# Performance work log

Measured on AMD Instinct MI355X. Metric: run time of the kernel, lower is better.

## Reference

```python
import jax, jax.numpy as jnp
import numpy as np

HEADS = 8
DIM_HEAD = 64
DIM = 512
MAX_POS_EMB = 512
SCALE = DIM_HEAD ** -0.5


def setup_inputs() -> dict:
    key = jax.random.key(0)
    ks = jax.random.split(key, 6)
    B, N = 2, 2048
    inner = HEADS * DIM_HEAD  # 512
    x = jax.random.normal(ks[0], (B, N, DIM), dtype=jnp.float32)
    # torch Linear weights stored as [out, in]; we keep [in, out] for x @ W
    Wq = jax.random.normal(ks[1], (DIM, inner), dtype=jnp.float32) * (DIM ** -0.5)
    Wkv = jax.random.normal(ks[2], (DIM, 2 * inner), dtype=jnp.float32) * (DIM ** -0.5)
    Wo = jax.random.normal(ks[3], (inner, DIM), dtype=jnp.float32) * (inner ** -0.5)
    bo = jax.random.normal(ks[4], (DIM,), dtype=jnp.float32) * 0.02
    rel_emb = jax.random.normal(ks[5], (2 * MAX_POS_EMB + 1, DIM_HEAD), dtype=jnp.float32)
    return {"x": x, "Wq": Wq, "Wkv": Wkv, "Wo": Wo, "bo": bo, "rel_emb": rel_emb}


def reference(x, Wq, Wkv, Wo, bo, rel_emb):
    B, N, _ = x.shape
    h, d = HEADS, DIM_HEAD
    q = x @ Wq                                # [B, N, h*d]
    kv = x @ Wkv                              # [B, N, 2*h*d]
    k, v = jnp.split(kv, 2, axis=-1)
    to_heads = lambda t: t.reshape(B, N, h, d).transpose(0, 2, 1, 3)  # [B, h, N, d]
    q, k, v = to_heads(q), to_heads(k), to_heads(v)

    dots = jnp.einsum('bhid,bhjd->bhij', q, k) * SCALE  # [B, h, N, N]

    # relative positional bias: dist clamped to [-max, max], shifted to [0, 2*max]
    seq = jnp.arange(N)
    dist = jnp.clip(seq[:, None] - seq[None, :], -MAX_POS_EMB, MAX_POS_EMB) + MAX_POS_EMB
    rel = rel_emb[dist]                                 # [N, N, d]
    pos_attn = jnp.einsum('bhnd,njd->bhnj', q, rel) * SCALE
    dots = dots + pos_attn

    attn = jax.nn.softmax(dots, axis=-1)
    out = jnp.einsum('bhij,bhjd->bhid', attn, v)        # [B, h, N, d]
    out = out.transpose(0, 2, 1, 3).reshape(B, N, h * d)
    return out @ Wo + bo
```

## Files before the change

kernel.cpp:

```cpp
#include <hip/hip_runtime.h>
#include <hip/hip_bf16.h>
#include <stdint.h>

#define HEADS 8
#define DHEAD 64
#define DIM 512
#define NSEQ 2048
#define BATCH 2
#define NROWS (BATCH * NSEQ)
#define QKV_N 1536
#define REL_ROWS 1025
#define REL_PITCH_ROWS 1088
#define NSPLIT 2
#define KV_PER_SPLIT (NSEQ / NSPLIT)

static constexpr float SCALE_LOG2E = 0.125f * 1.4426950408889634f;

typedef __attribute__((ext_vector_type(8))) short bf16x8;
typedef __attribute__((ext_vector_type(4))) float f32x4;

__device__ __forceinline__ uint16_t f2bf(float f) {
    union { float f; uint32_t u; } v{f};
    uint32_t r = (v.u + 0x7FFFu + ((v.u >> 16) & 1u)) >> 16;
    return (uint16_t)r;
}

__global__ void prep_all(const float* __restrict__ x, const float* __restrict__ rel,
                         const float* __restrict__ Wq, const float* __restrict__ Wkv,
                         const float* __restrict__ Wo,
                         uint16_t* __restrict__ xb, uint16_t* __restrict__ relb,
                         uint16_t* __restrict__ Wqkv_t, uint16_t* __restrict__ Wo_t) {
    if (blockIdx.x < 2048) {
        int total = NROWS * DIM + REL_PITCH_ROWS * DHEAD;
        for (int idx = blockIdx.x * blockDim.x + threadIdx.x; idx < total; idx += 2048 * blockDim.x) {
            if (idx < NROWS * DIM) {
                xb[idx] = f2bf(x[idx]);
            } else {
                int i2 = idx - NROWS * DIM;
                relb[i2] = (i2 < REL_ROWS * DHEAD) ? f2bf(rel[i2]) : (uint16_t)0;
            }
        }
        return;
    }
    __shared__ float tile[32][33];
    int bid = blockIdx.x - 2048;
    const float* src; uint16_t* dst; int J, ti, tj;
    if (bid < 256)      { src = Wq;  dst = Wqkv_t;             J = 512;  ti = bid >> 4;        tj = bid & 15; }
    else if (bid < 768) { int b = bid - 256; src = Wkv; dst = Wqkv_t + 512 * 512; J = 1024; ti = b >> 5; tj = b & 31; }
    else                { int b = bid - 768; src = Wo;  dst = Wo_t;   J = 512;  ti = b >> 4;        tj = b & 15; }
    int tx = threadIdx.x & 31, ty = threadIdx.x >> 5;
    int k0 = ti * 32, j0 = tj * 32;
    #pragma unroll
    for (int i = 0; i < 4; i++) tile[ty + 8 * i][tx] = src[(size_t)(k0 + ty + 8 * i) * J + j0 + tx];
    __syncthreads();
    #pragma unroll
    for (int i = 0; i < 4; i++) dst[(size_t)(j0 + ty + 8 * i) * 512 + k0 + tx] = f2bf(tile[tx][ty + 8 * i]);
}

template <bool BF16_OUT>
__global__ __launch_bounds__(256) void gemm128(const uint16_t* __restrict__ A,
                                               const uint16_t* __restrict__ Bt,
                                               void* __restrict__ Cout,
                                               const float* __restrict__ bias,
                                               int K, int ldc) {
    __shared__ char lds[32768];
    char* ldsA = lds;
    char* ldsB = lds + 16384;
    int m0 = blockIdx.x * 128, n0 = blockIdx.y * 128;
    int t = threadIdx.x, lane = t & 63, w = t >> 6;
    int wr = w >> 1, wc = w & 1;
    int l15 = lane & 15, lh = lane >> 4;
    f32x4 acc[4][4] = {};
    for (int k0 = 0; k0 < K; k0 += 64) {
        __syncthreads();
        {
            int row = t >> 3, ch = t & 7;
            #pragma unroll
            for (int p = 0; p < 4; p++) {
                int r = row + 32 * p;
                bf16x8 va = *(const bf16x8*)(A + (size_t)(m0 + r) * K + k0 + ch * 8);
                *(bf16x8*)(ldsA + r * 128 + ((ch * 16) ^ ((r & 7) << 4))) = va;
                bf16x8 vb = *(const bf16x8*)(Bt + (size_t)(n0 + r) * K + k0 + ch * 8);
                *(bf16x8*)(ldsB + r * 128 + ((ch * 16) ^ ((r & 7) << 4))) = vb;
            }
        }
        __syncthreads();
        #pragma unroll
        for (int kk = 0; kk < 2; kk++) {
            bf16x8 a[4], b[4];
            #pragma unroll
            for (int mi = 0; mi < 4; mi++) {
                int m = wr * 64 + mi * 16 + l15;
                a[mi] = *(const bf16x8*)(ldsA + m * 128 + ((kk * 64 + lh * 16) ^ ((m & 7) << 4)));
            }
            #pragma unroll
            for (int ni = 0; ni < 4; ni++) {
                int n = wc * 64 + ni * 16 + l15;
                b[ni] = *(const bf16x8*)(ldsB + n * 128 + ((kk * 64 + lh * 16) ^ ((n & 7) << 4)));
            }
            #pragma unroll
            for (int mi = 0; mi < 4; mi++)
                #pragma unroll
                for (int ni = 0; ni < 4; ni++)
                    acc[mi][ni] = __builtin_amdgcn_mfma_f32_16x16x32_bf16(a[mi], b[ni], acc[mi][ni], 0, 0, 0);
        }
    }
    #pragma unroll
    for (int mi = 0; mi < 4; mi++)
        #pragma unroll
        for (int ni = 0; ni < 4; ni++)
            #pragma unroll
            for (int i = 0; i < 4; i++) {
                int m = m0 + wr * 64 + mi * 16 + lh * 4 + i;
                int n = n0 + wc * 64 + ni * 16 + l15;
                float v = acc[mi][ni][i];
                if constexpr (BF16_OUT) ((uint16_t*)Cout)[(size_t)m * ldc + n] = f2bf(v);
                else                    ((float*)Cout)[(size_t)m * ldc + n] = v + bias[n];
            }
}

__global__ __launch_bounds__(512, 4) void attn_kernel(const uint16_t* __restrict__ QKV,
                                                      const uint16_t* __restrict__ relb,
                                                      float* __restrict__ Opart,
                                                      float* __restrict__ mlpart) {
    __shared__ __align__(16) char lds[53248];
    char* ldsQ = lds;
    char* ldsKV = lds + 16384;

    int flat = blockIdx.x + 16 * (blockIdx.y + 8 * blockIdx.z);
    int x = (flat & 7) * 64 + (flat >> 3);
    int qb = x & 15, h = (x >> 4) & 7, z = x >> 7;
    int b = z >> 1, sp = z & 1;

    int t = threadIdx.x, lane = t & 63, w = t >> 6;
    int l15 = lane & 15, lh = lane >> 4;
    int row = t >> 3, ch = t & 7;
    int n0 = qb * 128;
    int kvbase = sp * KV_PER_SPLIT;
    size_t rowQ = (size_t)b * NSEQ + n0;

    int swzSrc = (ch * 16) ^ ((row & 7) << 4);

    #pragma unroll
    for (int p = 0; p < 2; p++) {
        int r = row + 64 * p;
        const char* gsrc = (const char*)(QKV + (rowQ + r) * QKV_N + h * 64)
                           + ((ch * 16) ^ ((r & 7) << 4));
        __builtin_amdgcn_global_load_lds(gsrc, ldsQ + p * 8192 + t * 16, 16, 0, 0);
    }

    {
        int buf = t >> 8, idx = t & 255;
        uint32_t val = (idx < 16) ? 0x3F803F80u : 0u;
        char* p = ldsKV + buf * 18432 + 8192 + 8192 + (idx >> 4) * 128 + (idx & 15) * 8;
        *(uint32_t*)(p) = val;
        *(uint32_t*)(p + 4) = val;
    }

    auto stage_k = [&](int tile) {
        const char* gsrc = (const char*)(QKV + ((size_t)b * NSEQ + kvbase + tile * 64 + row) * QKV_N
                                         + 512 + h * 64) + swzSrc;
        __builtin_amdgcn_global_load_lds(gsrc, ldsKV + (tile & 1) * 18432 + t * 16, 16, 0, 0);
    };
    auto load_v = [&](int tile, bf16x8& vr) {
        vr = *(const bf16x8*)(QKV + ((size_t)b * NSEQ + kvbase + tile * 64 + row) * QKV_N
                              + 1024 + h * 64 + ch * 8);
    };
    auto scatter_v = [&](int tile, bf16x8& vr) {
        char* ldsV = ldsKV + (tile & 1) * 18432 + 8192;
        #pragma unroll
        for (int dd = 0; dd < 8; dd++) {
            int d = ch * 8 + dd;
            int s = dd ^ ch;
            *(uint16_t*)(ldsV + d * 128 + 2 * (row ^ (s << 3))) = (uint16_t)vr[dd];
        }
    };

    bf16x8 vr;
    stage_k(0);
    load_v(0, vr);
    scatter_v(0, vr);
    __syncthreads();

    bf16x8 qf[2];
    #pragma unroll
    for (int kk = 0; kk < 2; kk++) {
        int m = w * 16 + l15;
        qf[kk] = *(const bf16x8*)(ldsQ + m * 128 + ((kk * 64 + lh * 16) ^ ((m & 7) << 4)));
    }
    char* myP = ldsQ + w * 2048;

    f32x4 biasLo = {}, biasHi = {};
    {
        bf16x8 bl0 = *(const bf16x8*)(relb + lh * 8);
        bf16x8 bl1 = *(const bf16x8*)(relb + lh * 8 + 32);
        bf16x8 bh0 = *(const bf16x8*)(relb + 1024 * 64 + lh * 8);
        bf16x8 bh1 = *(const bf16x8*)(relb + 1024 * 64 + lh * 8 + 32);
        biasLo = __builtin_amdgcn_mfma_f32_16x16x32_bf16(qf[0], bl0, biasLo, 0, 0, 0);
        biasLo = __builtin_amdgcn_mfma_f32_16x16x32_bf16(qf[1], bl1, biasLo, 0, 0, 0);
        biasHi = __builtin_amdgcn_mfma_f32_16x16x32_bf16(qf[0], bh0, biasHi, 0, 0, 0);
        biasHi = __builtin_amdgcn_mfma_f32_16x16x32_bf16(qf[1], bh1, biasHi, 0, 0, 0);
    }

    f32x4 oacc[5] = {};
    float mrow[4];
    #pragma unroll
    for (int i = 0; i < 4; i++) mrow[i] = -INFINITY;

    int exAddr[4];
    #pragma unroll
    for (int i = 0; i < 4; i++)
        exAddr[i] = (((lane & 48) | ((lh * 4 + i + 15 - l15) & 15)) << 2);

    const int NT = KV_PER_SPLIT / 64;

    #pragma unroll 1
    for (int tt = 0; tt < NT; ++tt) {
        char* ldsK = ldsKV + (tt & 1) * 18432;
        char* ldsV = ldsK + 8192;
        if (tt > 0) __syncthreads();
        bool pf = (tt + 1 < NT);
        if (pf) {
            stage_k(tt + 1);
            load_v(tt + 1, vr);
        }

        int nk = n0 + w * 16 - (kvbase + tt * 64);
        bool fullLo = (nk <= -527), fullHi = (nk >= 575);

        f32x4 sacc[4] = {};
        __builtin_amdgcn_s_setprio(1);
        #pragma unroll
        for (int kk = 0; kk < 2; kk++)
            #pragma unroll
            for (int nf = 0; nf < 4; nf++) {
                int n = nf * 16 + l15;
                bf16x8 kfv = *(const bf16x8*)(ldsK + n * 128 + ((kk * 64 + lh * 16) ^ ((n & 7) << 4)));
                sacc[nf] = __builtin_amdgcn_mfma_f32_16x16x32_bf16(qf[kk], kfv, sacc[nf], 0, 0, 0);
            }
        __builtin_amdgcn_s_setprio(0);

        if (fullLo || fullHi) {
            f32x4 bc = fullLo ? biasLo : biasHi;
            #pragma unroll
            for (int nf = 0; nf < 4; nf++)
                #pragma unroll
                for (int i = 0; i < 4; i++)
                    sacc[nf][i] += bc[i];
        } else {
            int dlo = nk - 63;
            bf16x8 rfr[2][2];
            {
                int d = dlo + l15;
                d = d < -512 ? -512 : (d > 512 ? 512 : d);
                const uint16_t* rp = relb + (d + 512) * 64 + lh * 8;
                rfr[0][0] = *(const bf16x8*)(rp);
                rfr[0][1] = *(const bf16x8*)(rp + 32);
            }
            f32x4 rect[5] = {};
            #pragma unroll
            for (int f = 0; f < 5; f++) {
                if (f + 1 < 5) {
                    int d = dlo + (f + 1) * 16 + l15;
                    d = d < -512 ? -512 : (d > 512 ? 512 : d);
                    const uint16_t* rp = relb + (d + 512) * 64 + lh * 8;
                    rfr[(f + 1) & 1][0] = *(const bf16x8*)(rp);
                    rfr[(f + 1) & 1][1] = *(const bf16x8*)(rp + 32);
                }
                rect[f] = __builtin_amdgcn_mfma_f32_16x16x32_bf16(qf[0], rfr[f & 1][0], rect[f], 0, 0, 0);
                rect[f] = __builtin_amdgcn_mfma_f32_16x16x32_bf16(qf[1], rfr[f & 1][1], rect[f], 0, 0, 0);
                __builtin_amdgcn_sched_barrier(0);
            }
            #pragma unroll
            for (int i = 0; i < 4; i++) {
                bool hi = (l15 < lh * 4 + i);
                #pragma unroll
                for (int nf = 0; nf < 4; nf++) {
                    float v = hi ? rect[4 - nf][i] : rect[3 - nf][i];
                    union { float f; int s; } un{v};
                    un.s = __builtin_amdgcn_ds_bpermute(exAddr[i], un.s);
                    sacc[nf][i] += un.f;
                }
            }
        }

        float lmax = sacc[0][0];
        #pragma unroll
        for (int nf = 0; nf < 4; nf++)
            #pragma unroll
            for (int i = 0; i < 4; i++) lmax = fmaxf(lmax, sacc[nf][i]);
        float mmin = fminf(fminf(mrow[0], mrow[1]), fminf(mrow[2], mrow[3]));
        if (!__all(lmax <= mmin + 64.0f)) {
            #pragma unroll
            for (int i = 0; i < 4; i++) {
                float mx = fmaxf(fmaxf(sacc[0][i], sacc[1][i]), fmaxf(sacc[2][i], sacc[3][i]));
                mx = fmaxf(mx, __shfl_xor(mx, 1));
                mx = fmaxf(mx, __shfl_xor(mx, 2));
                mx = fmaxf(mx, __shfl_xor(mx, 4));
                mx = fmaxf(mx, __shfl_xor(mx, 8));
                float mnew = fmaxf(mrow[i], mx);
                float alpha = exp2f((mrow[i] - mnew) * SCALE_LOG2E);
                mrow[i] = mnew;
                #pragma unroll
                for (int nf = 0; nf < 5; nf++) oacc[nf][i] *= alpha;
            }
        }

        #pragma unroll
        for (int i = 0; i < 4; i++) {
            int r = lh * 4 + i;
            int rsw = (r & 7) << 4;
            #pragma unroll
            for (int nf = 0; nf < 4; nf++) {
                float p = exp2f((sacc[nf][i] - mrow[i]) * SCALE_LOG2E);
                uint32_t pb;
                asm("v_cvt_pk_bf16_f32 %0, %1, %2" : "=v"(pb) : "v"(p), "v"(p));
                *(uint16_t*)(myP + r * 128 + (((nf * 16 + l15) * 2) ^ rsw)) = (uint16_t)pb;
            }
        }

        asm volatile("s_waitcnt lgkmcnt(0)" ::: "memory");
        __builtin_amdgcn_sched_barrier(0);
        __builtin_amdgcn_s_setprio(1);
        #pragma unroll
        for (int kk = 0; kk < 2; kk++) {
            bf16x8 pa = *(const bf16x8*)(myP + l15 * 128 + ((kk * 64 + lh * 16) ^ ((l15 & 7) << 4)));
            #pragma unroll
            for (int nf = 0; nf < 5; nf++) {
                int d = nf * 16 + l15;
                int sd = (d & 7) ^ ((d >> 3) & 7);
                bf16x8 vb = *(const bf16x8*)(ldsV + d * 128 + 16 * ((kk * 4 + lh) ^ sd));
                oacc[nf] = __builtin_amdgcn_mfma_f32_16x16x32_bf16(pa, vb, oacc[nf], 0, 0, 0);
            }
        }
        __builtin_amdgcn_s_setprio(0);

        if (pf) scatter_v(tt + 1, vr);
        __syncthreads();
    }

    size_t rbase = ((size_t)(sp * BATCH + b) * HEADS + h) * NSEQ;
    #pragma unroll
    for (int nf = 0; nf < 4; nf++)
        #pragma unroll
        for (int i = 0; i < 4; i++) {
            int r = n0 + w * 16 + lh * 4 + i;
            Opart[(rbase + r) * 64 + nf * 16 + l15] = oacc[nf][i];
        }
    if (l15 == 0) {
        #pragma unroll
        for (int i = 0; i < 4; i++) {
            int r = n0 + w * 16 + lh * 4 + i;
            mlpart[(rbase + r) * 2]     = mrow[i];
            mlpart[(rbase + r) * 2 + 1] = oacc[4][i];
        }
    }
}

__global__ __launch_bounds__(256) void combine_kernel(const float* __restrict__ Opart,
                                                      const float* __restrict__ mlpart,
                                                      uint16_t* __restrict__ attO) {
    int lane = threadIdx.x & 63;
    int R = blockIdx.x * 4 + (threadIdx.x >> 6);
    const int SPSTRIDE = BATCH * HEADS * NSEQ;
    float m1 = mlpart[(size_t)R * 2], l1 = mlpart[(size_t)R * 2 + 1];
    float m2 = mlpart[((size_t)SPSTRIDE + R) * 2], l2 = mlpart[((size_t)SPSTRIDE + R) * 2 + 1];
    float M = fmaxf(m1, m2);
    float w1 = exp2f((m1 - M) * SCALE_LOG2E);
    float w2 = exp2f((m2 - M) * SCALE_LOG2E);
    float Linv = 1.f / (l1 * w1 + l2 * w2);
    float o1 = Opart[(size_t)R * 64 + lane];
    float o2 = Opart[((size_t)SPSTRIDE + R) * 64 + lane];
    float o = (o1 * w1 + o2 * w2) * Linv;
    int bh = R >> 11, n = R & 2047;
    int b = bh >> 3, hh = bh & 7;
    attO[((size_t)(b * NSEQ + n)) * DIM + hh * 64 + lane] = f2bf(o);
}

extern "C" void kernel_launch(void* const* d_in, const int* in_sizes, int n_in,
                              void* d_out, int out_size, void* d_ws, size_t ws_size,
                              hipStream_t stream) {
    const float* x   = (const float*)d_in[0];
    const float* Wq  = (const float*)d_in[1];
    const float* Wkv = (const float*)d_in[2];
    const float* Wo  = (const float*)d_in[3];
    const float* bo  = (const float*)d_in[4];
    const float* rel = (const float*)d_in[5];
    char* ws = (char*)d_ws;
    float*    mlp    = (float*)(ws);
    uint16_t* Wo_t   = (uint16_t*)(ws + 524288);
    uint16_t* relb   = (uint16_t*)(ws + 1048576);
    uint16_t* attO   = (uint16_t*)(ws + 1310720);
    uint16_t* QKV    = (uint16_t*)(ws + 5505024);
    float*    Opart  = (float*)(ws + 18087936);
    uint16_t* Xb     = (uint16_t*)(ws + 18087936);
    uint16_t* Wqkv_t = (uint16_t*)(ws + 22282240);

    prep_all<<<3072, 256, 0, stream>>>(x, rel, Wq, Wkv, Wo, Xb, relb, Wqkv_t, Wo_t);
    gemm128<true><<<dim3(32, 12), 256, 0, stream>>>(Xb, Wqkv_t, QKV, nullptr, 512, QKV_N);
    attn_kernel<<<dim3(16, 8, 4), 512, 0, stream>>>(QKV, relb, Opart, mlp);
    combine_kernel<<<8192, 256, 0, stream>>>(Opart, mlp, attO);
    gemm128<false><<<dim3(32, 4), 256, 0, stream>>>(attO, Wo_t, (float*)d_out, bo, 512, DIM);
}
```

Before: 134.0 us.

## Halve attention block to 64 query rows and single-buffer K/V tiles

The attention kernel now uses 256-thread blocks covering 64 query rows instead of 512 threads covering 128, which doubles the grid. K/V LDS staging goes from double-buffered to single-buffered, with the next tile's K load and V scatter issued after the end-of-iteration barrier. Together these cut LDS per block roughly in half, so more blocks can be resident per CU and there are more blocks to spread across the device. The cost is that each K/V tile is reused by fewer query rows, so global traffic rises, and the loss of double buffering exposes load latency within each iteration.

```diff
diff --git a/kernel.cpp b/kernel.cpp
--- a/kernel.cpp
+++ b/kernel.cpp
@@ -119,67 +119,70 @@
             }
 }
 
-__global__ __launch_bounds__(512, 4) void attn_kernel(const uint16_t* __restrict__ QKV,
+__global__ __launch_bounds__(256, 4) void attn_kernel(const uint16_t* __restrict__ QKV,
                                                       const uint16_t* __restrict__ relb,
                                                       float* __restrict__ Opart,
                                                       float* __restrict__ mlpart) {
-    __shared__ __align__(16) char lds[53248];
+    __shared__ __align__(16) char lds[26624];
     char* ldsQ = lds;
-    char* ldsKV = lds + 16384;
-
-    int flat = blockIdx.x + 16 * (blockIdx.y + 8 * blockIdx.z);
-    int x = (flat & 7) * 64 + (flat >> 3);
-    int qb = x & 15, h = (x >> 4) & 7, z = x >> 7;
+    char* ldsK = lds + 8192;
+    char* ldsV = lds + 16384;
+
+    int flat = blockIdx.x + 32 * (blockIdx.y + 8 * blockIdx.z);
+    int x = (flat & 7) * 128 + (flat >> 3);
+    int qb = x & 31, h = (x >> 5) & 7, z = x >> 8;
     int b = z >> 1, sp = z & 1;
 
     int t = threadIdx.x, lane = t & 63, w = t >> 6;
     int l15 = lane & 15, lh = lane >> 4;
-    int row = t >> 3, ch = t & 7;
-    int n0 = qb * 128;
+    int r4 = t >> 2, q4 = t & 3;
+    int n0 = qb * 64;
     int kvbase = sp * KV_PER_SPLIT;
-    size_t rowQ = (size_t)b * NSEQ + n0;
-
-    int swzSrc = (ch * 16) ^ ((row & 7) << 4);
 
     #pragma unroll
     for (int p = 0; p < 2; p++) {
-        int r = row + 64 * p;
-        const char* gsrc = (const char*)(QKV + (rowQ + r) * QKV_N + h * 64)
-                           + ((ch * 16) ^ ((r & 7) << 4));
-        __builtin_amdgcn_global_load_lds(gsrc, ldsQ + p * 8192 + t * 16, 16, 0, 0);
+        int r = p * 32 + (t >> 3);
+        const char* gsrc = (const char*)(QKV + ((size_t)b * NSEQ + n0 + r) * QKV_N + h * 64)
+                           + (((t & 7) * 16) ^ ((r & 7) << 4));
+        __builtin_amdgcn_global_load_lds(gsrc, ldsQ + p * 4096 + t * 16, 16, 0, 0);
     }
 
     {
-        int buf = t >> 8, idx = t & 255;
-        uint32_t val = (idx < 16) ? 0x3F803F80u : 0u;
-        char* p = ldsKV + buf * 18432 + 8192 + 8192 + (idx >> 4) * 128 + (idx & 15) * 8;
+        uint32_t val = ((t >> 4) == 0) ? 0x3F803F80u : 0u;
+        char* p = ldsV + 8192 + (t >> 4) * 128 + (t & 15) * 8;
         *(uint32_t*)(p) = val;
         *(uint32_t*)(p + 4) = val;
     }
 
     auto stage_k = [&](int tile) {
-        const char* gsrc = (const char*)(QKV + ((size_t)b * NSEQ + kvbase + tile * 64 + row) * QKV_N
-                                         + 512 + h * 64) + swzSrc;
-        __builtin_amdgcn_global_load_lds(gsrc, ldsKV + (tile & 1) * 18432 + t * 16, 16, 0, 0);
+        #pragma unroll
+        for (int p = 0; p < 2; p++) {
+            int r = p * 32 + (t >> 3);
+            const char* gsrc = (const char*)(QKV + ((size_t)b * NSEQ + kvbase + tile * 64 + r) * QKV_N
+                                             + 512 + h * 64) + (((t & 7) * 16) ^ ((r & 7) << 4));
+            __builtin_amdgcn_global_load_lds(gsrc, ldsK + p * 4096 + t * 16, 16, 0, 0);
+        }
     };
-    auto load_v = [&](int tile, bf16x8& vr) {
-        vr = *(const bf16x8*)(QKV + ((size_t)b * NSEQ + kvbase + tile * 64 + row) * QKV_N
-                              + 1024 + h * 64 + ch * 8);
+    auto load_v = [&](int tile, bf16x8* vr) {
+        size_t gro = ((size_t)b * NSEQ + kvbase + tile * 64 + r4) * QKV_N + 1024 + h * 64 + q4 * 16;
+        vr[0] = *(const bf16x8*)(QKV + gro);
+        vr[1] = *(const bf16x8*)(QKV + gro + 8);
     };
-    auto scatter_v = [&](int tile, bf16x8& vr) {
-        char* ldsV = ldsKV + (tile & 1) * 18432 + 8192;
-        #pragma unroll
-        for (int dd = 0; dd < 8; dd++) {
-            int d = ch * 8 + dd;
-            int s = dd ^ ch;
-            *(uint16_t*)(ldsV + d * 128 + 2 * (row ^ (s << 3))) = (uint16_t)vr[dd];
-        }
+    auto scatter_v = [&](bf16x8* vr) {
+        #pragma unroll
+        for (int p = 0; p < 2; p++)
+            #pragma unroll
+            for (int dd = 0; dd < 8; dd++) {
+                int d = q4 * 16 + p * 8 + dd;
+                int s = (d & 7) ^ (d >> 3);
+                *(uint16_t*)(ldsV + d * 128 + 2 * (r4 ^ (s << 3))) = (uint16_t)vr[p][dd];
+            }
     };
 
-    bf16x8 vr;
+    bf16x8 vr[2];
     stage_k(0);
     load_v(0, vr);
-    scatter_v(0, vr);
+    scatter_v(vr);
     __syncthreads();
 
     bf16x8 qf[2];
@@ -216,14 +219,9 @@
 
     #pragma unroll 1
     for (int tt = 0; tt < NT; ++tt) {
-        char* ldsK = ldsKV + (tt & 1) * 18432;
-        char* ldsV = ldsK + 8192;
         if (tt > 0) __syncthreads();
         bool pf = (tt + 1 < NT);
-        if (pf) {
-            stage_k(tt + 1);
-            load_v(tt + 1, vr);
-        }
+        if (pf) load_v(tt + 1, vr);
 
         int nk = n0 + w * 16 - (kvbase + tt * 64);
         bool fullLo = (nk <= -527), fullHi = (nk >= 575);
@@ -335,8 +333,8 @@
         }
         __builtin_amdgcn_s_setprio(0);
 
-        if (pf) scatter_v(tt + 1, vr);
         __syncthreads();
+        if (pf) { stage_k(tt + 1); scatter_v(vr); }
     }
 
     size_t rbase = ((size_t)(sp * BATCH + b) * HEADS + h) * NSEQ;
@@ -398,7 +396,7 @@
 
     prep_all<<<3072, 256, 0, stream>>>(x, rel, Wq, Wkv, Wo, Xb, relb, Wqkv_t, Wo_t);
     gemm128<true><<<dim3(32, 12), 256, 0, stream>>>(Xb, Wqkv_t, QKV, nullptr, 512, QKV_N);
-    attn_kernel<<<dim3(16, 8, 4), 512, 0, stream>>>(QKV, relb, Opart, mlp);
+    attn_kernel<<<dim3(32, 8, 4), 256, 0, stream>>>(QKV, relb, Opart, mlp);
     combine_kernel<<<8192, 256, 0, stream>>>(Opart, mlp, attO);
     gemm128<false><<<dim3(32, 4), 256, 0, stream>>>(attO, Wo_t, (float*)d_out, bo, 512, DIM);
 }
```

Result: slower. 183.9 us (+37.3%).
